# Performance work log

Hardware: AMD Instinct MI355X
Metric: run time of the kernel (lower is better)

## Reference

```python
import jax, jax.numpy as jnp
import numpy as np

B, N, DIM = 8, 1024, 1024
HEADS, DIM_HEAD = 16, 64
INNER = HEADS * DIM_HEAD  # 1024


def setup_inputs() -> dict:
    key = jax.random.key(0)
    k1, k2, k3 = jax.random.split(key, 3)
    x = jax.random.normal(k1, (B, N, DIM), dtype=jnp.float32)
    # Dense kernels (Glorot-ish scale for numerical sanity)
    w_qkv = jax.random.normal(k2, (DIM, 3 * INNER), dtype=jnp.float32) * (DIM ** -0.5)
    w_out = jax.random.normal(k3, (INNER, DIM), dtype=jnp.float32) * (INNER ** -0.5)
    b_out = jnp.zeros((DIM,), dtype=jnp.float32)
    return {"x": x, "w_qkv": w_qkv, "w_out": w_out, "b_out": b_out}


def reference(x, w_qkv, w_out, b_out):
    scale = DIM_HEAD ** -0.5
    qkv = x @ w_qkv                                   # [B, N, 3*INNER]
    q, k, v = jnp.split(qkv, 3, axis=-1)              # each [B, N, INNER]

    def to_heads(t):
        # [B, N, H*Dh] -> [B, H, N, Dh]
        return t.reshape(B, N, HEADS, DIM_HEAD).transpose(0, 2, 1, 3)

    q, k, v = to_heads(q), to_heads(k), to_heads(v)
    dots = jnp.einsum("bhid,bhjd->bhij", q, k) * scale   # [B, H, N, N]
    attn = jax.nn.softmax(dots, axis=-1)
    out = jnp.einsum("bhij,bhjd->bhid", attn, v)          # [B, H, N, Dh]
    out = out.transpose(0, 2, 1, 3).reshape(B, N, INNER)  # merge heads
    return out @ w_out + b_out                            # project_out (dropout inactive at inference)
```

## Files before the change

kernel.cpp:

```cpp
#include <hip/hip_runtime.h>
#include <hip/hip_bf16.h>
#include <math.h>

typedef __bf16 bf16_t;
typedef __bf16 bf16x4 __attribute__((ext_vector_type(4)));
typedef __bf16 bf16x8 __attribute__((ext_vector_type(8)));
typedef float f32x4 __attribute__((ext_vector_type(4)));

#define LOG2E 1.44269504088896340736f

#define GL2LDS(g, l)                                                     \
  __builtin_amdgcn_global_load_lds(                                      \
      (const __attribute__((address_space(1))) unsigned int*)(g),        \
      (__attribute__((address_space(3))) unsigned int*)(l), 16, 0, 0)

__global__ __launch_bounds__(256) void convert_f32_bf16(const float* __restrict__ in,
                                                        bf16_t* __restrict__ out) {
  const size_t idx = (size_t)(blockIdx.x * 256 + threadIdx.x) * 8;
  f32x4 a = *(const f32x4*)&in[idx];
  f32x4 b = *(const f32x4*)&in[idx + 4];
  bf16x8 v;
#pragma unroll
  for (int i = 0; i < 4; i++) { v[i] = (bf16_t)a[i]; v[i + 4] = (bf16_t)b[i]; }
  *(bf16x8*)&out[idx] = v;
}

__global__ __launch_bounds__(256) void transpose_f32_bf16(const float* __restrict__ in,
                                                          bf16_t* __restrict__ out,
                                                          int R, int C) {
  __shared__ bf16_t t[64][65];
  const int c0 = blockIdx.x * 64, r0 = blockIdx.y * 64;
  const int tx = threadIdx.x, ty = threadIdx.y;
#pragma unroll
  for (int i = 0; i < 16; i++) {
    int r = ty + i * 4;
    t[r][tx] = (bf16_t)in[(size_t)(r0 + r) * C + c0 + tx];
  }
  __syncthreads();
#pragma unroll
  for (int i = 0; i < 16; i++) {
    int r = ty + i * 4;
    out[(size_t)(c0 + r) * R + r0 + tx] = t[tx][r];
  }
}

template <int MODE>
__global__ __launch_bounds__(256) void gemm128(const bf16_t* __restrict__ A,
                                               const bf16_t* __restrict__ Bt,
                                               bf16_t* __restrict__ Qb,
                                               bf16_t* __restrict__ Kb,
                                               bf16_t* __restrict__ Vtb,
                                               const float* __restrict__ bias,
                                               float* __restrict__ Out) {
  constexpr int K = 1024;
  __shared__ __align__(16) bf16_t As[128 * 64];
  __shared__ __align__(16) bf16_t Bs[128 * 64];
  const int m0 = blockIdx.y * 128, n0 = blockIdx.x * 128;
  const int tid = threadIdx.x;
  const int w = tid >> 6, l = tid & 63;
  const int lr = l & 15, lq = l >> 4;
  const int lrx = lr & 7;
  const int wm = (w & 1) * 64, wn = (w >> 1) * 64;
  const int sR[4] = {(0 * 256 + tid) >> 3, (1 * 256 + tid) >> 3,
                     (2 * 256 + tid) >> 3, (3 * 256 + tid) >> 3};
  int sC[4];
#pragma unroll
  for (int i = 0; i < 4; i++) sC[i] = ((tid & 7) ^ (sR[i] & 7)) * 8;
  f32x4 acc[4][4] = {};

  for (int k0 = 0; k0 < K; k0 += 64) {
#pragma unroll
    for (int i = 0; i < 4; i++) {
      const int ldsoff = (i * 256 + w * 64) * 8;
      GL2LDS(&A[(size_t)(m0 + sR[i]) * K + k0 + sC[i]], &As[ldsoff]);
      GL2LDS(&Bt[(size_t)(n0 + sR[i]) * K + k0 + sC[i]], &Bs[ldsoff]);
    }
    __syncthreads();
#pragma unroll
    for (int ks = 0; ks < 2; ks++) {
      const int g = ks * 4 + lq;
      const int sw = ((g ^ lrx) << 3);
      bf16x8 af[4], bfr[4];
#pragma unroll
      for (int mt = 0; mt < 4; mt++)
        af[mt] = *(const bf16x8*)&As[((wm + mt * 16 + lr) << 6) + sw];
#pragma unroll
      for (int nt = 0; nt < 4; nt++)
        bfr[nt] = *(const bf16x8*)&Bs[((wn + nt * 16 + lr) << 6) + sw];
#pragma unroll
      for (int mt = 0; mt < 4; mt++)
#pragma unroll
        for (int nt = 0; nt < 4; nt++)
          acc[mt][nt] = __builtin_amdgcn_mfma_f32_16x16x32_bf16(af[mt], bfr[nt],
                                                                acc[mt][nt], 0, 0, 0);
    }
    __syncthreads();
  }

#pragma unroll
  for (int mt = 0; mt < 4; mt++)
#pragma unroll
    for (int nt = 0; nt < 4; nt++)
#pragma unroll
      for (int i = 0; i < 4; i++) {
        int m = m0 + wm + mt * 16 + lq * 4 + i;
        int c = n0 + wn + nt * 16 + lr;
        float v = acc[mt][nt][i];
        if (MODE == 1) {
          Out[(size_t)m * 1024 + c] = v + bias[c];
        } else {
          int b = m >> 10, n = m & 1023;
          int which = c >> 10, cc = c & 1023;
          int hh = cc >> 6, d = cc & 63;
          size_t qk = ((size_t)((b * 16 + hh) * 1024 + n)) * 64 + d;
          if (which == 0)
            Qb[qk] = (bf16_t)(v * (0.125f * LOG2E));
          else if (which == 1)
            Kb[qk] = (bf16_t)v;
          else
            Vtb[((size_t)((b * 16 + hh) * 64 + d)) * 1024 + n] = (bf16_t)v;
        }
      }
}

#define KVS 68
#define PS  72
__global__ __launch_bounds__(256) void attn128(const bf16_t* __restrict__ Qb,
                                               const bf16_t* __restrict__ Kb,
                                               const bf16_t* __restrict__ Vtb,
                                               bf16_t* __restrict__ Ob) {
  __shared__ __align__(16) bf16_t Ks[2][64 * KVS];
  __shared__ __align__(16) bf16_t Vs[2][64 * KVS];
  __shared__ __align__(16) bf16_t Pl[4 * 32 * PS];
  const int bid = blockIdx.x;
  const int qt = bid & 7, h = (bid >> 3) & 15, b = bid >> 7;
  const bf16_t* Qh = Qb + (size_t)((b * 16 + h) * 1024) * 64;
  const bf16_t* Kh = Kb + (size_t)((b * 16 + h) * 1024) * 64;
  const bf16_t* Vh = Vtb + (size_t)((b * 16 + h) * 64) * 1024;
  const int tid = threadIdx.x, w = tid >> 6, l = tid & 63;
  const int lr = l & 15, lq = l >> 4;
  const int q0 = qt * 128 + w * 32;

  bf16x8 onesf;
#pragma unroll
  for (int i = 0; i < 8; i++) onesf[i] = (lr == 0) ? (bf16_t)1.0f : (bf16_t)0.0f;

  const int sr = tid >> 3, sc = tid & 7;

  bf16x8 qf[2][2];
#pragma unroll
  for (int mt = 0; mt < 2; mt++)
#pragma unroll
    for (int ks = 0; ks < 2; ks++)
      qf[mt][ks] = *(const bf16x8*)&Qh[(size_t)(q0 + mt * 16 + lr) * 64 + ks * 32 + lq * 8];

  {
    bf16x8 k0 = *(const bf16x8*)&Kh[(size_t)sr * 64 + sc * 8];
    bf16x8 k1 = *(const bf16x8*)&Kh[(size_t)(sr + 32) * 64 + sc * 8];
    bf16x8 v0 = *(const bf16x8*)&Vh[(size_t)sr * 1024 + sc * 8];
    bf16x8 v1 = *(const bf16x8*)&Vh[(size_t)(sr + 32) * 1024 + sc * 8];
    *(bf16x8*)&Ks[0][sr * KVS + sc * 8] = k0;
    *(bf16x8*)&Ks[0][(sr + 32) * KVS + sc * 8] = k1;
    *(bf16x8*)&Vs[0][sr * KVS + sc * 8] = v0;
    *(bf16x8*)&Vs[0][(sr + 32) * KVS + sc * 8] = v1;
  }
  __syncthreads();

  f32x4 o[2][4] = {};
  f32x4 o5[2] = {};
  bf16_t* pw = &Pl[w * 32 * PS];

  for (int it = 0; it < 16; ++it) {
    const int buf = it & 1;
    bf16x8 nk0, nk1, nv0, nv1;
    if (it < 15) {
      const int jn = (it + 1) * 64;
      nk0 = *(const bf16x8*)&Kh[(size_t)(jn + sr) * 64 + sc * 8];
      nk1 = *(const bf16x8*)&Kh[(size_t)(jn + sr + 32) * 64 + sc * 8];
      nv0 = *(const bf16x8*)&Vh[(size_t)sr * 1024 + jn + sc * 8];
      nv1 = *(const bf16x8*)&Vh[(size_t)(sr + 32) * 1024 + jn + sc * 8];
    }
    f32x4 s[2][4] = {};
#pragma unroll
    for (int ks = 0; ks < 2; ks++)
#pragma unroll
      for (int nt = 0; nt < 4; nt++) {
        bf16x8 kf = *(const bf16x8*)&Ks[buf][(nt * 16 + lr) * KVS + ks * 32 + lq * 8];
#pragma unroll
        for (int mt = 0; mt < 2; mt++)
          s[mt][nt] = __builtin_amdgcn_mfma_f32_16x16x32_bf16(qf[mt][ks], kf, s[mt][nt], 0, 0, 0);
      }
#pragma unroll
    for (int mt = 0; mt < 2; mt++)
#pragma unroll
      for (int nt = 0; nt < 4; nt++)
#pragma unroll
        for (int i = 0; i < 4; i++)
          pw[(mt * 16 + lq * 4 + i) * PS + nt * 16 + lr] = (bf16_t)exp2f(s[mt][nt][i]);
#pragma unroll
    for (int ks = 0; ks < 2; ks++) {
      bf16x8 af[2];
#pragma unroll
      for (int mt = 0; mt < 2; mt++)
        af[mt] = *(const bf16x8*)&pw[(mt * 16 + lr) * PS + ks * 32 + lq * 8];
#pragma unroll
      for (int nt = 0; nt < 4; nt++) {
        bf16x8 vf = *(const bf16x8*)&Vs[buf][(nt * 16 + lr) * KVS + ks * 32 + lq * 8];
#pragma unroll
        for (int mt = 0; mt < 2; mt++)
          o[mt][nt] = __builtin_amdgcn_mfma_f32_16x16x32_bf16(af[mt], vf, o[mt][nt], 0, 0, 0);
      }
#pragma unroll
      for (int mt = 0; mt < 2; mt++)
        o5[mt] = __builtin_amdgcn_mfma_f32_16x16x32_bf16(af[mt], onesf, o5[mt], 0, 0, 0);
    }
    if (it < 15) {
      *(bf16x8*)&Ks[buf ^ 1][sr * KVS + sc * 8] = nk0;
      *(bf16x8*)&Ks[buf ^ 1][(sr + 32) * KVS + sc * 8] = nk1;
      *(bf16x8*)&Vs[buf ^ 1][sr * KVS + sc * 8] = nv0;
      *(bf16x8*)&Vs[buf ^ 1][(sr + 32) * KVS + sc * 8] = nv1;
    }
    __syncthreads();
  }
#pragma unroll
  for (int mt = 0; mt < 2; mt++)
#pragma unroll
    for (int i = 0; i < 4; i++) {
      float lsum = __shfl(o5[mt][i], lq * 16);
      float inv = 1.0f / lsum;
      int grow = b * 1024 + q0 + mt * 16 + lq * 4 + i;
#pragma unroll
      for (int nt = 0; nt < 4; nt++) {
        int col = h * 64 + nt * 16 + lr;
        Ob[(size_t)grow * 1024 + col] = (bf16_t)(o[mt][nt][i] * inv);
      }
    }
}

extern "C" void kernel_launch(void* const* d_in, const int* in_sizes, int n_in,
                              void* d_out, int out_size, void* d_ws, size_t ws_size,
                              hipStream_t stream) {
  const float* x     = (const float*)d_in[0];
  const float* w_qkv = (const float*)d_in[1];
  const float* w_out = (const float*)d_in[2];
  const float* b_out = (const float*)d_in[3];
  float* out = (float*)d_out;

  bf16_t* ws = (bf16_t*)d_ws;
  const size_t SZ = (size_t)8 * 1024 * 1024;
  bf16_t* Qb  = ws;
  bf16_t* Kb  = Qb + SZ;
  bf16_t* Vtb = Kb + SZ;
  bf16_t* Ob  = Vtb + SZ;
  bf16_t* Wqt = Ob + SZ;
  bf16_t* Wot = Wqt + (size_t)3072 * 1024;
  bf16_t* Xb  = Ob;

  hipLaunchKernelGGL(convert_f32_bf16, dim3(4096), dim3(256), 0, stream, x, Xb);
  hipLaunchKernelGGL(transpose_f32_bf16, dim3(48, 16), dim3(64, 4), 0, stream,
                     w_qkv, Wqt, 1024, 3072);
  hipLaunchKernelGGL(transpose_f32_bf16, dim3(16, 16), dim3(64, 4), 0, stream,
                     w_out, Wot, 1024, 1024);
  hipLaunchKernelGGL((gemm128<0>), dim3(24, 64), dim3(256), 0, stream,
                     Xb, Wqt, Qb, Kb, Vtb, (const float*)nullptr, (float*)nullptr);
  hipLaunchKernelGGL(attn128, dim3(1024), dim3(256), 0, stream, Qb, Kb, Vtb, Ob);
  hipLaunchKernelGGL((gemm128<1>), dim3(8, 64), dim3(256), 0, stream,
                     Ob, Wot, (bf16_t*)nullptr, (bf16_t*)nullptr, (bf16_t*)nullptr,
                     b_out, out);
}
```

Before: 283.5 us.

## Replace 128x128 GEMM with double-buffered 256x256 pipelined GEMM using 8 waves

Both projection GEMMs now use 256x256 tiles with 512 threads, holding 8x4 MFMA fragments per wave. The K loop is split into half-tile phases with double-buffered LDS, and global-to-LDS loads for later k-steps are issued while the current ones compute. Explicit vmcnt waits, raw barriers and setprio around the MFMA bursts replace the old load-sync-compute-sync loop. This aims to hide memory latency and raise data reuse per tile, at the cost of 128KB LDS, more registers, and fewer blocks (384 and 128), which may leave CUs idle in the output projection.

```diff
diff --git a/kernel.cpp b/kernel.cpp
--- a/kernel.cpp
+++ b/kernel.cpp
@@ -3,7 +3,6 @@
 #include <math.h>
 
 typedef __bf16 bf16_t;
-typedef __bf16 bf16x4 __attribute__((ext_vector_type(4)));
 typedef __bf16 bf16x8 __attribute__((ext_vector_type(8)));
 typedef float f32x4 __attribute__((ext_vector_type(4)));
 
@@ -13,6 +12,14 @@
   __builtin_amdgcn_global_load_lds(                                      \
       (const __attribute__((address_space(1))) unsigned int*)(g),        \
       (__attribute__((address_space(3))) unsigned int*)(l), 16, 0, 0)
+
+#define BAR() asm volatile("s_barrier" ::: "memory")
+#define VMCNT(n) asm volatile("s_waitcnt vmcnt(" #n ")" ::: "memory")
+#define LGKM0()                                         \
+  do {                                                  \
+    asm volatile("s_waitcnt lgkmcnt(0)" ::: "memory");  \
+    __builtin_amdgcn_sched_barrier(0);                  \
+  } while (0)
 
 __global__ __launch_bounds__(256) void convert_f32_bf16(const float* __restrict__ in,
                                                         bf16_t* __restrict__ out) {
@@ -45,74 +52,117 @@
 }
 
 template <int MODE>
-__global__ __launch_bounds__(256) void gemm128(const bf16_t* __restrict__ A,
-                                               const bf16_t* __restrict__ Bt,
-                                               bf16_t* __restrict__ Qb,
-                                               bf16_t* __restrict__ Kb,
-                                               bf16_t* __restrict__ Vtb,
-                                               const float* __restrict__ bias,
-                                               float* __restrict__ Out) {
+__global__ __launch_bounds__(512, 2) void gemm256(const bf16_t* __restrict__ A,
+                                                  const bf16_t* __restrict__ Bt,
+                                                  bf16_t* __restrict__ Qb,
+                                                  bf16_t* __restrict__ Kb,
+                                                  bf16_t* __restrict__ Vtb,
+                                                  const float* __restrict__ bias,
+                                                  float* __restrict__ Out) {
   constexpr int K = 1024;
-  __shared__ __align__(16) bf16_t As[128 * 64];
-  __shared__ __align__(16) bf16_t Bs[128 * 64];
-  const int m0 = blockIdx.y * 128, n0 = blockIdx.x * 128;
+  constexpr int NT = K / 64;
+  __shared__ __align__(16) bf16_t As[2][2][256 * 32];
+  __shared__ __align__(16) bf16_t Bs[2][2][256 * 32];
+  const int m0 = blockIdx.y * 256, n0 = blockIdx.x * 256;
   const int tid = threadIdx.x;
   const int w = tid >> 6, l = tid & 63;
   const int lr = l & 15, lq = l >> 4;
-  const int lrx = lr & 7;
-  const int wm = (w & 1) * 64, wn = (w >> 1) * 64;
-  const int sR[4] = {(0 * 256 + tid) >> 3, (1 * 256 + tid) >> 3,
-                     (2 * 256 + tid) >> 3, (3 * 256 + tid) >> 3};
-  int sC[4];
-#pragma unroll
-  for (int i = 0; i < 4; i++) sC[i] = ((tid & 7) ^ (sR[i] & 7)) * 8;
-  f32x4 acc[4][4] = {};
-
-  for (int k0 = 0; k0 < K; k0 += 64) {
-#pragma unroll
-    for (int i = 0; i < 4; i++) {
-      const int ldsoff = (i * 256 + w * 64) * 8;
-      GL2LDS(&A[(size_t)(m0 + sR[i]) * K + k0 + sC[i]], &As[ldsoff]);
-      GL2LDS(&Bt[(size_t)(n0 + sR[i]) * K + k0 + sC[i]], &Bs[ldsoff]);
-    }
-    __syncthreads();
-#pragma unroll
-    for (int ks = 0; ks < 2; ks++) {
-      const int g = ks * 4 + lq;
-      const int sw = ((g ^ lrx) << 3);
-      bf16x8 af[4], bfr[4];
-#pragma unroll
-      for (int mt = 0; mt < 4; mt++)
-        af[mt] = *(const bf16x8*)&As[((wm + mt * 16 + lr) << 6) + sw];
-#pragma unroll
-      for (int nt = 0; nt < 4; nt++)
-        bfr[nt] = *(const bf16x8*)&Bs[((wn + nt * 16 + lr) << 6) + sw];
-#pragma unroll
-      for (int mt = 0; mt < 4; mt++)
-#pragma unroll
-        for (int nt = 0; nt < 4; nt++)
-          acc[mt][nt] = __builtin_amdgcn_mfma_f32_16x16x32_bf16(af[mt], bfr[nt],
-                                                                acc[mt][nt], 0, 0, 0);
-    }
-    __syncthreads();
-  }
-
-#pragma unroll
-  for (int mt = 0; mt < 4; mt++)
-#pragma unroll
-    for (int nt = 0; nt < 4; nt++)
+  const int wm = w >> 2, wn = w & 3;
+
+  const int r0s = tid >> 2, p0s = tid & 3;
+  const int r1s = r0s + 128;
+  const int c20 = p0s ^ ((r0s >> 3) & 3);
+  const int c21 = p0s ^ ((r1s >> 3) & 3);
+  const size_t gA0 = (size_t)(m0 + r0s) * K + c20 * 8;
+  const size_t gA1 = (size_t)(m0 + r1s) * K + c21 * 8;
+  const size_t gB0 = (size_t)(n0 + r0s) * K + c20 * 8;
+  const size_t gB1 = (size_t)(n0 + r1s) * K + c21 * 8;
+  const int ldsu0 = (w * 64) * 8;
+  const int ldsu1 = (512 + w * 64) * 8;
+
+#define STG_A(bf_, ks_, kt_)                                  \
+  do {                                                        \
+    const size_t kk_ = (size_t)(kt_) * 64 + (ks_) * 32;       \
+    GL2LDS(&A[gA0 + kk_], &As[bf_][ks_][ldsu0]);              \
+    GL2LDS(&A[gA1 + kk_], &As[bf_][ks_][ldsu1]);              \
+  } while (0)
+#define STG_B(bf_, ks_, kt_)                                  \
+  do {                                                        \
+    const size_t kk_ = (size_t)(kt_) * 64 + (ks_) * 32;       \
+    GL2LDS(&Bt[gB0 + kk_], &Bs[bf_][ks_][ldsu0]);             \
+    GL2LDS(&Bt[gB1 + kk_], &Bs[bf_][ks_][ldsu1]);             \
+  } while (0)
+
+  int aoff[8], boff[4];
+#pragma unroll
+  for (int mf = 0; mf < 8; mf++) {
+    const int row = wm * 128 + mf * 16 + lr;
+    aoff[mf] = row * 32 + ((lq ^ ((row >> 3) & 3)) << 3);
+  }
+#pragma unroll
+  for (int nf = 0; nf < 4; nf++) {
+    const int row = wn * 64 + nf * 16 + lr;
+    boff[nf] = row * 32 + ((lq ^ ((row >> 3) & 3)) << 3);
+  }
+
+  f32x4 acc[8][4] = {};
+
+  STG_A(0, 0, 0);
+  STG_B(0, 0, 0);
+  STG_A(0, 1, 0);
+  STG_B(0, 1, 0);
+  STG_A(1, 0, 1);
+  STG_B(1, 0, 1);
+  VMCNT(8);
+  BAR();
+
+#define PHASE(g_, ks_, STAGE_STMT, TAIL_STMT)                                  \
+  {                                                                            \
+    bf16x8 af[4], bv[4];                                                       \
+    _Pragma("unroll") for (int mf = 0; mf < 4; mf++)                           \
+        af[mf] = *(const bf16x8*)&As[buf][ks_][aoff[(g_) * 4 + mf]];           \
+    _Pragma("unroll") for (int nf = 0; nf < 4; nf++)                           \
+        bv[nf] = *(const bf16x8*)&Bs[buf][ks_][boff[nf]];                      \
+    STAGE_STMT;                                                                \
+    BAR();                                                                     \
+    LGKM0();                                                                   \
+    __builtin_amdgcn_s_setprio(1);                                             \
+    _Pragma("unroll") for (int mf = 0; mf < 4; mf++)                           \
+        _Pragma("unroll") for (int nf = 0; nf < 4; nf++)                       \
+            acc[(g_) * 4 + mf][nf] = __builtin_amdgcn_mfma_f32_16x16x32_bf16(  \
+                af[mf], bv[nf], acc[(g_) * 4 + mf][nf], 0, 0, 0);              \
+    __builtin_amdgcn_s_setprio(0);                                             \
+    TAIL_STMT;                                                                 \
+    BAR();                                                                     \
+  }
+
+  for (int t = 0; t < NT; ++t) {
+    const int buf = t & 1;
+    PHASE(0, 0, if (t + 1 < NT) STG_A(buf ^ 1, 1, t + 1), );
+    PHASE(1, 0, if (t + 1 < NT) STG_B(buf ^ 1, 1, t + 1),
+          if (t == NT - 1) { VMCNT(0); } else { VMCNT(8); });
+    PHASE(0, 1, if (t + 2 < NT) STG_A(buf, 0, t + 2), );
+    PHASE(1, 1, if (t + 2 < NT) STG_B(buf, 0, t + 2),
+          if (t == NT - 2) { VMCNT(4); } else if (t < NT - 2) { VMCNT(8); });
+  }
+#undef PHASE
+
+#pragma unroll
+  for (int mf = 0; mf < 8; mf++)
+#pragma unroll
+    for (int nf = 0; nf < 4; nf++)
 #pragma unroll
       for (int i = 0; i < 4; i++) {
-        int m = m0 + wm + mt * 16 + lq * 4 + i;
-        int c = n0 + wn + nt * 16 + lr;
-        float v = acc[mt][nt][i];
+        const int m = m0 + wm * 128 + mf * 16 + lq * 4 + i;
+        const int c = n0 + wn * 64 + nf * 16 + lr;
+        const float v = acc[mf][nf][i];
         if (MODE == 1) {
           Out[(size_t)m * 1024 + c] = v + bias[c];
         } else {
-          int b = m >> 10, n = m & 1023;
-          int which = c >> 10, cc = c & 1023;
-          int hh = cc >> 6, d = cc & 63;
-          size_t qk = ((size_t)((b * 16 + hh) * 1024 + n)) * 64 + d;
+          const int b = m >> 10, n = m & 1023;
+          const int which = c >> 10, cc = c & 1023;
+          const int hh = cc >> 6, d = cc & 63;
+          const size_t qk = ((size_t)((b * 16 + hh) * 1024 + n)) * 64 + d;
           if (which == 0)
             Qb[qk] = (bf16_t)(v * (0.125f * LOG2E));
           else if (which == 1)
@@ -261,10 +311,10 @@
                      w_qkv, Wqt, 1024, 3072);
   hipLaunchKernelGGL(transpose_f32_bf16, dim3(16, 16), dim3(64, 4), 0, stream,
                      w_out, Wot, 1024, 1024);
-  hipLaunchKernelGGL((gemm128<0>), dim3(24, 64), dim3(256), 0, stream,
+  hipLaunchKernelGGL((gemm256<0>), dim3(12, 32), dim3(512), 0, stream,
                      Xb, Wqt, Qb, Kb, Vtb, (const float*)nullptr, (float*)nullptr);
   hipLaunchKernelGGL(attn128, dim3(1024), dim3(256), 0, stream, Qb, Kb, Vtb, Ob);
-  hipLaunchKernelGGL((gemm128<1>), dim3(8, 64), dim3(256), 0, stream,
+  hipLaunchKernelGGL((gemm256<1>), dim3(4, 32), dim3(512), 0, stream,
                      Ob, Wot, (bf16_t*)nullptr, (bf16_t*)nullptr, (bf16_t*)nullptr,
                      b_out, out);
 }
```

Result: slower. 308.9 us (+9.0%).

## Double-buffer GEMM with 128x256 tiles, 512 threads and global-to-LDS prefetch

Applied to the files above, without the earlier changes.

Rewrites the projection GEMM to use a 128x256 block tile with 8 waves and a double-buffered LDS pipeline with K-step 32. The next tile is prefetched through global_load_lds while MFMAs run on the current buffer. It uses raw s_barrier/waitcnt and setprio around the MFMA burst. This is meant to hide global memory latency and cut barrier stalls, at the cost of a smaller K step per sync and fewer blocks (768 and 256) in flight across the CUs.

```diff
diff --git a/kernel.cpp b/kernel.cpp
--- a/kernel.cpp
+++ b/kernel.cpp
@@ -3,7 +3,6 @@
 #include <math.h>
 
 typedef __bf16 bf16_t;
-typedef __bf16 bf16x4 __attribute__((ext_vector_type(4)));
 typedef __bf16 bf16x8 __attribute__((ext_vector_type(8)));
 typedef float f32x4 __attribute__((ext_vector_type(4)));
 
@@ -13,6 +12,14 @@
   __builtin_amdgcn_global_load_lds(                                      \
       (const __attribute__((address_space(1))) unsigned int*)(g),        \
       (__attribute__((address_space(3))) unsigned int*)(l), 16, 0, 0)
+
+#define BAR() asm volatile("s_barrier" ::: "memory")
+#define VMCNT0() asm volatile("s_waitcnt vmcnt(0)" ::: "memory")
+#define LGKM0()                                         \
+  do {                                                  \
+    asm volatile("s_waitcnt lgkmcnt(0)" ::: "memory");  \
+    __builtin_amdgcn_sched_barrier(0);                  \
+  } while (0)
 
 __global__ __launch_bounds__(256) void convert_f32_bf16(const float* __restrict__ in,
                                                         bf16_t* __restrict__ out) {
@@ -45,74 +52,96 @@
 }
 
 template <int MODE>
-__global__ __launch_bounds__(256) void gemm128(const bf16_t* __restrict__ A,
-                                               const bf16_t* __restrict__ Bt,
-                                               bf16_t* __restrict__ Qb,
-                                               bf16_t* __restrict__ Kb,
-                                               bf16_t* __restrict__ Vtb,
-                                               const float* __restrict__ bias,
-                                               float* __restrict__ Out) {
+__global__ __launch_bounds__(512, 2) void gemmT(const bf16_t* __restrict__ A,
+                                                const bf16_t* __restrict__ Bt,
+                                                bf16_t* __restrict__ Qb,
+                                                bf16_t* __restrict__ Kb,
+                                                bf16_t* __restrict__ Vtb,
+                                                const float* __restrict__ bias,
+                                                float* __restrict__ Out) {
   constexpr int K = 1024;
-  __shared__ __align__(16) bf16_t As[128 * 64];
-  __shared__ __align__(16) bf16_t Bs[128 * 64];
-  const int m0 = blockIdx.y * 128, n0 = blockIdx.x * 128;
+  constexpr int NT = K / 32;
+  __shared__ __align__(16) bf16_t As[2][128 * 32];
+  __shared__ __align__(16) bf16_t Bs[2][256 * 32];
+  const int m0 = blockIdx.y * 128, n0 = blockIdx.x * 256;
   const int tid = threadIdx.x;
   const int w = tid >> 6, l = tid & 63;
   const int lr = l & 15, lq = l >> 4;
-  const int lrx = lr & 7;
-  const int wm = (w & 1) * 64, wn = (w >> 1) * 64;
-  const int sR[4] = {(0 * 256 + tid) >> 3, (1 * 256 + tid) >> 3,
-                     (2 * 256 + tid) >> 3, (3 * 256 + tid) >> 3};
-  int sC[4];
-#pragma unroll
-  for (int i = 0; i < 4; i++) sC[i] = ((tid & 7) ^ (sR[i] & 7)) * 8;
+  const int wm = w >> 2, wn = w & 3;
+
+  const int rs = tid >> 2, ps = tid & 3;
+  const int cs = (ps ^ ((rs >> 1) & 3)) * 8;
+  const size_t gA  = (size_t)(m0 + rs) * K + cs;
+  const size_t gB0 = (size_t)(n0 + rs) * K + cs;
+  const size_t gB1 = (size_t)(n0 + rs + 128) * K + cs;
+  const int ldsu0 = (w * 64) * 8;
+  const int ldsu1 = (512 + w * 64) * 8;
+
+#define STG(bf_, kt_)                                   \
+  do {                                                  \
+    const size_t kk_ = (size_t)(kt_) * 32;              \
+    GL2LDS(&A[gA + kk_], &As[bf_][ldsu0]);              \
+    GL2LDS(&Bt[gB0 + kk_], &Bs[bf_][ldsu0]);            \
+    GL2LDS(&Bt[gB1 + kk_], &Bs[bf_][ldsu1]);            \
+  } while (0)
+
+  int aoff[4], boff[4];
+#pragma unroll
+  for (int mf = 0; mf < 4; mf++) {
+    const int row = wm * 64 + mf * 16 + lr;
+    aoff[mf] = row * 32 + ((lq ^ ((row >> 1) & 3)) << 3);
+  }
+#pragma unroll
+  for (int nf = 0; nf < 4; nf++) {
+    const int row = wn * 64 + nf * 16 + lr;
+    boff[nf] = row * 32 + ((lq ^ ((row >> 1) & 3)) << 3);
+  }
+
   f32x4 acc[4][4] = {};
 
-  for (int k0 = 0; k0 < K; k0 += 64) {
-#pragma unroll
-    for (int i = 0; i < 4; i++) {
-      const int ldsoff = (i * 256 + w * 64) * 8;
-      GL2LDS(&A[(size_t)(m0 + sR[i]) * K + k0 + sC[i]], &As[ldsoff]);
-      GL2LDS(&Bt[(size_t)(n0 + sR[i]) * K + k0 + sC[i]], &Bs[ldsoff]);
-    }
-    __syncthreads();
-#pragma unroll
-    for (int ks = 0; ks < 2; ks++) {
-      const int g = ks * 4 + lq;
-      const int sw = ((g ^ lrx) << 3);
-      bf16x8 af[4], bfr[4];
-#pragma unroll
-      for (int mt = 0; mt < 4; mt++)
-        af[mt] = *(const bf16x8*)&As[((wm + mt * 16 + lr) << 6) + sw];
-#pragma unroll
-      for (int nt = 0; nt < 4; nt++)
-        bfr[nt] = *(const bf16x8*)&Bs[((wn + nt * 16 + lr) << 6) + sw];
-#pragma unroll
-      for (int mt = 0; mt < 4; mt++)
-#pragma unroll
-        for (int nt = 0; nt < 4; nt++)
-          acc[mt][nt] = __builtin_amdgcn_mfma_f32_16x16x32_bf16(af[mt], bfr[nt],
-                                                                acc[mt][nt], 0, 0, 0);
-    }
-    __syncthreads();
-  }
-
-#pragma unroll
-  for (int mt = 0; mt < 4; mt++)
-#pragma unroll
-    for (int nt = 0; nt < 4; nt++)
+  STG(0, 0);
+  VMCNT0();
+  BAR();
+
+  for (int t = 0; t < NT; ++t) {
+    const int buf = t & 1;
+    if (t + 1 < NT) STG(buf ^ 1, t + 1);
+    bf16x8 af[4], bv[4];
+#pragma unroll
+    for (int mf = 0; mf < 4; mf++)
+      af[mf] = *(const bf16x8*)&As[buf][aoff[mf]];
+#pragma unroll
+    for (int nf = 0; nf < 4; nf++)
+      bv[nf] = *(const bf16x8*)&Bs[buf][boff[nf]];
+    LGKM0();
+    __builtin_amdgcn_s_setprio(1);
+#pragma unroll
+    for (int mf = 0; mf < 4; mf++)
+#pragma unroll
+      for (int nf = 0; nf < 4; nf++)
+        acc[mf][nf] = __builtin_amdgcn_mfma_f32_16x16x32_bf16(af[mf], bv[nf],
+                                                              acc[mf][nf], 0, 0, 0);
+    __builtin_amdgcn_s_setprio(0);
+    VMCNT0();
+    BAR();
+  }
+
+#pragma unroll
+  for (int mf = 0; mf < 4; mf++)
+#pragma unroll
+    for (int nf = 0; nf < 4; nf++)
 #pragma unroll
       for (int i = 0; i < 4; i++) {
-        int m = m0 + wm + mt * 16 + lq * 4 + i;
-        int c = n0 + wn + nt * 16 + lr;
-        float v = acc[mt][nt][i];
+        const int m = m0 + wm * 64 + mf * 16 + lq * 4 + i;
+        const int c = n0 + wn * 64 + nf * 16 + lr;
+        const float v = acc[mf][nf][i];
         if (MODE == 1) {
           Out[(size_t)m * 1024 + c] = v + bias[c];
         } else {
-          int b = m >> 10, n = m & 1023;
-          int which = c >> 10, cc = c & 1023;
-          int hh = cc >> 6, d = cc & 63;
-          size_t qk = ((size_t)((b * 16 + hh) * 1024 + n)) * 64 + d;
+          const int b = m >> 10, n = m & 1023;
+          const int which = c >> 10, cc = c & 1023;
+          const int hh = cc >> 6, d = cc & 63;
+          const size_t qk = ((size_t)((b * 16 + hh) * 1024 + n)) * 64 + d;
           if (which == 0)
             Qb[qk] = (bf16_t)(v * (0.125f * LOG2E));
           else if (which == 1)
@@ -261,10 +290,10 @@
                      w_qkv, Wqt, 1024, 3072);
   hipLaunchKernelGGL(transpose_f32_bf16, dim3(16, 16), dim3(64, 4), 0, stream,
                      w_out, Wot, 1024, 1024);
-  hipLaunchKernelGGL((gemm128<0>), dim3(24, 64), dim3(256), 0, stream,
+  hipLaunchKernelGGL((gemmT<0>), dim3(12, 64), dim3(512), 0, stream,
                      Xb, Wqt, Qb, Kb, Vtb, (const float*)nullptr, (float*)nullptr);
   hipLaunchKernelGGL(attn128, dim3(1024), dim3(256), 0, stream, Qb, Kb, Vtb, Ob);
-  hipLaunchKernelGGL((gemm128<1>), dim3(8, 64), dim3(256), 0, stream,
+  hipLaunchKernelGGL((gemmT<1>), dim3(4, 64), dim3(512), 0, stream,
                      Ob, Wot, (bf16_t*)nullptr, (bf16_t*)nullptr, (bf16_t*)nullptr,
                      b_out, out);
 }
```

Result: slower. 303.9 us (+7.2%).
